# Kernel optimization log

Measured on AMD Instinct MI355X. Metric: run time of the kernel, lower is better.

Reference implementation:

```python
import jax, jax.numpy as jnp
import numpy as np

P = 4          # patch_size
LAM = 0.5      # init_lambda
B, C, H, W = 8, 96, 128, 128

def _dct_mat(N):
    # torch_dct unnormalized DCT-II matrix: D[k,n] = 2*cos(pi*(2n+1)k/(2N))
    n = np.arange(N)
    return 2.0 * np.cos(np.pi * (2.0 * n[None, :] + 1.0) * n[:, None] / (2.0 * N))

_D = jnp.asarray(_dct_mat(P), dtype=jnp.float32)
_Di = jnp.asarray(np.linalg.inv(_dct_mat(P)), dtype=jnp.float32)  # exact inverse -> idct(dct(x)) == x

def _dct2(x):
    # DCT-II over last two dims of [..., P, P]
    return jnp.einsum('ij,...jk,lk->...il', _D, x, _D)

def _idct2(x):
    return jnp.einsum('ij,...jk,lk->...il', _Di, x, _Di)

def _conv3x3(x, w, b):
    y = jax.lax.conv_general_dilated(x, w, (1, 1), 'SAME',
                                     dimension_numbers=('NCHW', 'OIHW', 'NCHW'))
    return y + b[None, :, None, None]

def setup_inputs() -> dict:
    key = jax.random.key(0)
    ks = jax.random.split(key, 5)
    std = 1.0 / np.sqrt(C * 9)
    return {
        'input1': jax.random.normal(ks[0], (B, C, H, W), jnp.float32),
        'input2': jax.random.normal(ks[1], (B, C, H, W), jnp.float32),
        'wq': jax.random.normal(ks[2], (C, C, 3, 3), jnp.float32) * std,
        'bq': jnp.zeros((C,), jnp.float32),
        'wk': jax.random.normal(ks[3], (C, C, 3, 3), jnp.float32) * std,
        'bk': jnp.zeros((C,), jnp.float32),
        'wv': jax.random.normal(ks[4], (C, C, 3, 3), jnp.float32) * std,
        'bv': jnp.zeros((C,), jnp.float32),
        'temperature': jnp.ones((1, 1), jnp.float32),
    }

def reference(input1, input2, wq, bq, wk, bk, wv, bv, temperature):
    b, c, h, w = input1.shape
    F_Q = _conv3x3(input1, wq, bq)
    F_K = _conv3x3(input1, wk, bk)
    F_V = _conv3x3(input2, wv, bv)
    hp, wp = h // P, w // P
    # 'b c (h p1) (w p2) -> b c h w p1 p2'
    to_patch = lambda x: x.reshape(b, c, hp, P, wp, P).transpose(0, 1, 2, 4, 3, 5)
    fft_Q = _dct2(to_patch(F_Q))          # [b,c,hp,wp,P,P]
    fft_K = _dct2(to_patch(F_K))
    F1 = jnp.matmul(fft_Q, fft_K)         # per-patch PxP matmul
    L = hp * wp * P * P                   # == h*w
    F1f = F1.reshape(b, c, L)
    Fq = fft_Q.reshape(b, c, L)
    Fk = fft_K.reshape(b, c, L)
    # channel-channel attention: [b,c,L] @ [b,L,c] -> [b,c,c]
    attn = jnp.einsum('bil,bjl->bij', Fq, Fk) * temperature[0, 0]
    attn = jax.nn.softmax(attn, axis=-1)
    Fcfr = jnp.einsum('bij,bjl->bil', attn, F1f).reshape(b, c, hp, wp, P, P)
    Fcfr_out = _idct2(Fcfr)
    # 'b c h w p1 p2 -> b c (h p1) (w p2)'
    Fcfrout = Fcfr_out.transpose(0, 1, 2, 4, 3, 5).reshape(b, c, h, w)
    out1 = jnp.matmul(Fcfrout, F_V)       # batched HxW matmul (H==W)
    Fdfr = F_V - out1 * LAM
    return jnp.matmul(Fcfrout, F_Q) + Fdfr
```

## Files before the change

### kernel.cpp

```cpp
#include <hip/hip_runtime.h>

typedef unsigned short u16;
typedef unsigned int u32;
typedef __bf16 bf16x8 __attribute__((ext_vector_type(8)));
typedef float f32x4 __attribute__((ext_vector_type(4)));
typedef int i32x4 __attribute__((ext_vector_type(4)));

#define BATCH 8
#define CH 96
#define HWSZ 16384
#define PADP (130*130*96)

#define OFF_FQ     0ULL
#define OFF_FK     50331648ULL
#define OFF_GT     50331648ULL
#define OFF_FVN    75497472ULL
#define OFF_PAD1H  100663296ULL
#define OFF_F1W    100663296ULL
#define OFF_PART   126621696ULL
#define OFF_PAD1L  126621696ULL
#define OFF_PAD2   152580096ULL
#define OFF_FCFR   152580096ULL
#define OFF_FVB    178538496ULL
#define OFF_ATTNB  203704320ULL
#define OFF_WQK    203851776ULL
#define OFF_WV     204515328ULL
#define WS_NEED    204681216ULL

__device__ __forceinline__ u16 f2bf(float f) {
    u32 u = __builtin_bit_cast(u32, f);
    u += 0x7fffu + ((u >> 16) & 1u);
    return (u16)(u >> 16);
}
__device__ __forceinline__ float bf2f(u16 h) {
    u32 u = ((u32)h) << 16;
    return __builtin_bit_cast(float, u);
}
__device__ __forceinline__ f32x4 mfma16(i32x4 a, i32x4 b, f32x4 c) {
    return __builtin_amdgcn_mfma_f32_16x16x32_bf16(
        __builtin_bit_cast(bf16x8, a), __builtin_bit_cast(bf16x8, b), c, 0, 0, 0);
}
__device__ __forceinline__ void gl_lds16(const u16* g, u16* l) {
    __builtin_amdgcn_global_load_lds(
        (const __attribute__((address_space(1))) unsigned int*)g,
        (__attribute__((address_space(3))) unsigned int*)l, 16, 0, 0);
}

__global__ __launch_bounds__(256) void k_diag(float* __restrict__ out, int n, float val) {
    for (int i = blockIdx.x * 256 + threadIdx.x; i < n; i += gridDim.x * 256) out[i] = val;
}

__global__ __launch_bounds__(256) void k_zhalo(u16* __restrict__ p) {
    size_t base = (size_t)blockIdx.x * PADP;
    for (int i = threadIdx.x; i < 130 * 96; i += 256) {
        p[base + i] = 0;
        p[base + (size_t)129 * 130 * 96 + i] = 0;
    }
    for (int i = threadIdx.x; i < 128 * 2 * 96; i += 256) {
        int row = i / 192, k = i - row * 192;
        int x = (k < 96) ? 0 : 129, c = (k < 96) ? k : k - 96;
        p[base + ((size_t)(row + 1) * 130 + x) * 96 + c] = 0;
    }
}

__global__ __launch_bounds__(256) void k_trans_split(const float* __restrict__ src,
        u16* __restrict__ dh, u16* __restrict__ dl) {
    __shared__ float tile[96][129];
    int b = blockIdx.x >> 7, y = blockIdx.x & 127;
    const float* s = src + (size_t)b * CH * HWSZ + (size_t)y * 128;
    for (int idx = threadIdx.x; idx < CH * 128; idx += 256) {
        int c = idx >> 7, x = idx & 127;
        tile[c][x] = s[(size_t)c * HWSZ + x];
    }
    __syncthreads();
    size_t obase = ((size_t)(b * 130 + y + 1) * 130 + 1) * 96;
    for (int idx = threadIdx.x; idx < 128 * CH; idx += 256) {
        int x = idx / CH, c = idx - x * CH;
        float v = tile[c][x];
        u16 h = f2bf(v);
        dh[obase + idx] = h;
        if (dl) dl[obase + idx] = f2bf(v - bf2f(h));
    }
}

__global__ __launch_bounds__(128) void k_weights_all(const float* __restrict__ wq,
        const float* __restrict__ wk, const float* __restrict__ wv,
        u16* __restrict__ dqk, u16* __restrict__ dv) {
    int co = blockIdx.x;
    if (co < 192) {
        const float* w = (co < 96) ? wq : wk;
        int cs = (co < 96) ? co : co - 96;
        for (int idx = threadIdx.x; idx < 864; idx += 128) {
            int tap = idx / 96, ci = idx - tap * 96;
            int cic = ci >> 5, g = (ci >> 3) & 3, c7 = ci & 7;
            float v = w[((size_t)cs * 96 + ci) * 9 + tap];
            u16 h = f2bf(v), lo = f2bf(v - bf2f(h));
            size_t s = (size_t)(cic * 9 + tap);
            dqk[(((s * 2 + 0) * 4 + g) * 192 + co) * 8 + c7] = h;
            dqk[(((s * 2 + 1) * 4 + g) * 192 + co) * 8 + c7] = lo;
        }
    } else {
        int cs = co - 192;
        for (int idx = threadIdx.x; idx < 864; idx += 128) {
            int tap = idx / 96, ci = idx - tap * 96;
            int cic = ci >> 5, g = (ci >> 3) & 3, c7 = ci & 7;
            float v = wv[((size_t)cs * 96 + ci) * 9 + tap];
            size_t s = (size_t)(cic * 9 + tap);
            dv[((s * 4 + g) * 96 + cs) * 8 + c7] = f2bf(v);
        }
    }
}

__global__ __launch_bounds__(512, 4) void k_convqk6h(
        const u16* __restrict__ ph, const u16* __restrict__ pl,
        const u16* __restrict__ wqk,
        const float* __restrict__ bq, const float* __restrict__ bk,
        float* __restrict__ fq, float* __restrict__ fk, int bbase) {
    __shared__ u16 wbuf[2][12288];
    const int tid = threadIdx.x;
    const int wg = ((blockIdx.x & 7) << 6) | (blockIdx.x >> 3);
    const int b = bbase + (wg >> 7), y = wg & 127;
    const int w = tid >> 6, lane = tid & 63, l15 = lane & 15, g = lane >> 4;
    const int wx = w & 3, wc = w >> 2;
    f32x4 acc[2][6];
#pragma unroll
    for (int mf = 0; mf < 2; mf++)
#pragma unroll
        for (int f = 0; f < 6; f++) acc[mf][f] = (f32x4){0.f, 0.f, 0.f, 0.f};
    {
#pragma unroll
        for (int j = 0; j < 3; j++)
            gl_lds16(wqk + (size_t)(tid + j * 512) * 8, &wbuf[0][(size_t)(tid + j * 512) * 8]);
    }
    i32x4 ah0, ah1, al0, al1;
    {
        size_t ab = ((size_t)(b * 130 + y) * 130 + (wx * 32 + l15)) * 96 + g * 8;
        ah0 = *(const i32x4*)(ph + ab);
        ah1 = *(const i32x4*)(ph + ab + 16 * 96);
        al0 = *(const i32x4*)(pl + ab);
        al1 = *(const i32x4*)(pl + ab + 16 * 96);
    }
    __syncthreads();
    for (int s = 0; s < 27; s++) {
        const int cur = s & 1;
        i32x4 nh0, nh1, nl0, nl1;
        if (s + 1 < 27) {
            const u16* src = wqk + (size_t)(s + 1) * 12288;
#pragma unroll
            for (int j = 0; j < 3; j++)
                gl_lds16(src + (size_t)(tid + j * 512) * 8, &wbuf[cur ^ 1][(size_t)(tid + j * 512) * 8]);
            const int s1 = s + 1;
            const int cic1 = s1 / 9, tap1 = s1 - cic1 * 9;
            const int dy1 = tap1 / 3 - 1, dx1 = tap1 - (tap1 / 3) * 3 - 1;
            size_t ab = ((size_t)(b * 130 + y + 1 + dy1) * 130 + (wx * 32 + l15 + 1 + dx1)) * 96
                      + cic1 * 32 + g * 8;
            nh0 = *(const i32x4*)(ph + ab);
            nh1 = *(const i32x4*)(ph + ab + 16 * 96);
            nl0 = *(const i32x4*)(pl + ab);
            nl1 = *(const i32x4*)(pl + ab + 16 * 96);
        }
#pragma unroll
        for (int f = 0; f < 6; f++) {
            const int cob = wc * 96 + f * 16 + l15;
            i32x4 bh = *(const i32x4*)(&wbuf[cur][((0 + g) * 192 + cob) * 8]);
            i32x4 bl = *(const i32x4*)(&wbuf[cur][((4 + g) * 192 + cob) * 8]);
            acc[0][f] = mfma16(ah0, bh, acc[0][f]);
            acc[0][f] = mfma16(ah0, bl, acc[0][f]);
            acc[0][f] = mfma16(al0, bh, acc[0][f]);
            acc[1][f] = mfma16(ah1, bh, acc[1][f]);
            acc[1][f] = mfma16(ah1, bl, acc[1][f]);
            acc[1][f] = mfma16(al1, bh, acc[1][f]);
        }
        __syncthreads();
        if (s + 1 < 27) { ah0 = nh0; ah1 = nh1; al0 = nl0; al1 = nl1; }
    }
    const float* bias = wc ? bk : bq;
    float* op = wc ? fk : fq;
#pragma unroll
    for (int f = 0; f < 6; f++) {
        const int co = f * 16 + l15;
        const float bb = bias[co];
#pragma unroll
        for (int mf = 0; mf < 2; mf++) {
            const int xp = wx * 32 + mf * 16 + g * 4;
#pragma unroll
            for (int r = 0; r < 4; r++)
                op[((size_t)((b * 128 + y) * 128 + xp + r)) * 96 + co] = acc[mf][f][r] + bb;
        }
    }
}

__global__ __launch_bounds__(512, 4) void k_convqk7h(
        const u16* __restrict__ ph, const u16* __restrict__ pl,
        const u16* __restrict__ wqk,
        const float* __restrict__ bq, const float* __restrict__ bk,
        float* __restrict__ fq, float* __restrict__ fk, int bbase) {
    __shared__ u16 wbuf[2][12288];
    const int tid = threadIdx.x;
    const int wg = ((blockIdx.x & 7) << 6) | (blockIdx.x >> 3);
    const int b = bbase + (wg >> 7), y = wg & 127;
    const int w = tid >> 6, lane = tid & 63, l15 = lane & 15, g = lane >> 4;
    const int qk = w >> 2, coh = (w >> 1) & 1, xh = w & 1;
    const int cob = qk * 96 + coh * 48;
    f32x4 acc[4][3];
#pragma unroll
    for (int mf = 0; mf < 4; mf++)
#pragma unroll
        for (int f = 0; f < 3; f++) acc[mf][f] = (f32x4){0.f, 0.f, 0.f, 0.f};
    {
#pragma unroll
        for (int j = 0; j < 3; j++)
            gl_lds16(wqk + (size_t)(tid + j * 512) * 8, &wbuf[0][(size_t)(tid + j * 512) * 8]);
    }
    i32x4 ah[4], al[4];
    {
        size_t ab = ((size_t)(b * 130 + y) * 130 + (xh * 64 + l15)) * 96 + g * 8;
#pragma unroll
        for (int mf = 0; mf < 4; mf++) {
            ah[mf] = *(const i32x4*)(ph + ab + (size_t)mf * 16 * 96);
            al[mf] = *(const i32x4*)(pl + ab + (size_t)mf * 16 * 96);
        }
    }
    __syncthreads();
    for (int s = 0; s < 27; s++) {
        const int cur = s & 1;
        i32x4 nah[4], nal[4];
        if (s + 1 < 27) {
            const u16* src = wqk + (size_t)(s + 1) * 12288;
#pragma unroll
            for (int j = 0; j < 3; j++)
                gl_lds16(src + (size_t)(tid + j * 512) * 8, &wbuf[cur ^ 1][(size_t)(tid + j * 512) * 8]);
            const int s1 = s + 1;
            const int cic1 = s1 / 9, tap1 = s1 - cic1 * 9;
            const int dy1 = tap1 / 3 - 1, dx1 = tap1 - (tap1 / 3) * 3 - 1;
            size_t ab1 = ((size_t)(b * 130 + y + 1 + dy1) * 130 + (xh * 64 + l15 + 1 + dx1)) * 96
                       + cic1 * 32 + g * 8;
#pragma unroll
            for (int mf = 0; mf < 4; mf++) {
                nah[mf] = *(const i32x4*)(ph + ab1 + (size_t)mf * 16 * 96);
                nal[mf] = *(const i32x4*)(pl + ab1 + (size_t)mf * 16 * 96);
            }
        }
#pragma unroll
        for (int f = 0; f < 3; f++) {
            const int cw = cob + f * 16 + l15;
            i32x4 bh = *(const i32x4*)(&wbuf[cur][((0 + g) * 192 + cw) * 8]);
            i32x4 bl = *(const i32x4*)(&wbuf[cur][((4 + g) * 192 + cw) * 8]);
#pragma unroll
            for (int mf = 0; mf < 4; mf++) {
                acc[mf][f] = mfma16(ah[mf], bh, acc[mf][f]);
                acc[mf][f] = mfma16(ah[mf], bl, acc[mf][f]);
                acc[mf][f] = mfma16(al[mf], bh, acc[mf][f]);
            }
        }
        __syncthreads();
        if (s + 1 < 27) {
#pragma unroll
            for (int mf = 0; mf < 4; mf++) { ah[mf] = nah[mf]; al[mf] = nal[mf]; }
        }
    }
    const float* bias = qk ? bk : bq;
    float* op = qk ? fk : fq;
#pragma unroll
    for (int f = 0; f < 3; f++) {
        const int co = coh * 48 + f * 16 + l15;
        const float bb = bias[co];
#pragma unroll
        for (int mf = 0; mf < 4; mf++) {
            const int xp = xh * 64 + mf * 16 + g * 4;
#pragma unroll
            for (int r = 0; r < 4; r++)
                op[((size_t)((b * 128 + y) * 128 + xp + r)) * 96 + co] = acc[mf][f][r] + bb;
        }
    }
}

__global__ __launch_bounds__(512, 4) void k_convv6(
        const u16* __restrict__ p2, const u16* __restrict__ wv,
        const float* __restrict__ bv, u16* __restrict__ fvb) {
    __shared__ u16 vbuf[2][3072];
    const int tid = threadIdx.x;
    const int wg = ((blockIdx.x & 7) << 7) | (blockIdx.x >> 3);
    const int b = wg >> 7, y = wg & 127;
    const int w = tid >> 6, lane = tid & 63, l15 = lane & 15, g = lane >> 4;
    const int wx = w & 3, wc = w >> 2;
    f32x4 acc[2][3];
#pragma unroll
    for (int mf = 0; mf < 2; mf++)
#pragma unroll
        for (int f = 0; f < 3; f++) acc[mf][f] = (f32x4){0.f, 0.f, 0.f, 0.f};
    if (tid < 384)
        gl_lds16(wv + (size_t)tid * 8, &vbuf[0][(size_t)tid * 8]);
    i32x4 ah0, ah1;
    {
        size_t ab = ((size_t)(b * 130 + y) * 130 + (wx * 32 + l15)) * 96 + g * 8;
        ah0 = *(const i32x4*)(p2 + ab);
        ah1 = *(const i32x4*)(p2 + ab + 16 * 96);
    }
    __syncthreads();
    for (int s = 0; s < 27; s++) {
        const int cur = s & 1;
        i32x4 nh0, nh1;
        if (s + 1 < 27) {
            if (tid < 384)
                gl_lds16(wv + (size_t)(s + 1) * 3072 + (size_t)tid * 8, &vbuf[cur ^ 1][(size_t)tid * 8]);
            const int s1 = s + 1;
            const int cic1 = s1 / 9, tap1 = s1 - cic1 * 9;
            const int dy1 = tap1 / 3 - 1, dx1 = tap1 - (tap1 / 3) * 3 - 1;
            size_t ab = ((size_t)(b * 130 + y + 1 + dy1) * 130 + (wx * 32 + l15 + 1 + dx1)) * 96
                      + cic1 * 32 + g * 8;
            nh0 = *(const i32x4*)(p2 + ab);
            nh1 = *(const i32x4*)(p2 + ab + 16 * 96);
        }
#pragma unroll
        for (int f = 0; f < 3; f++) {
            const int cof = wc * 48 + f * 16 + l15;
            i32x4 bfr = *(const i32x4*)(&vbuf[cur][(g * 96 + cof) * 8]);
            acc[0][f] = mfma16(ah0, bfr, acc[0][f]);
            acc[1][f] = mfma16(ah1, bfr, acc[1][f]);
        }
        __syncthreads();
        if (s + 1 < 27) { ah0 = nh0; ah1 = nh1; }
    }
#pragma unroll
    for (int f = 0; f < 3; f++) {
        const int co = wc * 48 + f * 16 + l15;
        const float bb = bv[co];
#pragma unroll
        for (int mf = 0; mf < 2; mf++) {
            const int xp = wx * 32 + mf * 16 + g * 4;
#pragma unroll
            for (int r = 0; r < 4; r++)
                fvb[((size_t)((b * 128 + y) * 128 + xp + r)) * 96 + co] = f2bf(acc[mf][f][r] + bb);
        }
    }
}

__global__ __launch_bounds__(256) void k_pattn2(
        const float* __restrict__ fq, const float* __restrict__ fk,
        u16* __restrict__ f1w, float* __restrict__ part) {
    __shared__ float qs[96 * 65];
    __shared__ float ks[96 * 65];
    int blk = blockIdx.x;
    int b = blk >> 7, ys = (blk >> 2) & 31, xq = blk & 3;
    int y0 = ys * 4, x0 = xq * 32;
    int tx = threadIdx.x & 15, ty = threadIdx.x >> 4;
    double accD[6][6];
#pragma unroll
    for (int a = 0; a < 6; a++)
#pragma unroll
        for (int bb = 0; bb < 6; bb++) accD[a][bb] = 0.0;
#pragma unroll
    for (int cx = 0; cx < 2; cx++) {
        for (int idx = threadIdx.x; idx < 1536; idx += 256) {
            int p = idx / 24, c0 = (idx - p * 24) * 4;
            int ry = p >> 4, rx = p & 15;
            size_t off = ((size_t)((b * 128 + y0 + ry) * 128 + x0 + cx * 16 + rx)) * 96 + c0;
            f32x4 qv = *(const f32x4*)(fq + off);
            f32x4 kv = *(const f32x4*)(fk + off);
#pragma unroll
            for (int u = 0; u < 4; u++) {
                qs[(c0 + u) * 65 + p] = qv[u];
                ks[(c0 + u) * 65 + p] = kv[u];
            }
        }
        __syncthreads();
        for (int item = threadIdx.x; item < 384; item += 256) {
            int j = item / 96, c = item - j * 96;
            float A[4][4], Bm[4][4];
#pragma unroll
            for (int r = 0; r < 4; r++)
#pragma unroll
                for (int m = 0; m < 4; m++) {
                    A[r][m] = qs[c * 65 + r * 16 + j * 4 + m];
                    Bm[r][m] = ks[c * 65 + r * 16 + j * 4 + m];
                }
            float rsB[4], csB[4], rsA[4], tot = 0.f;
#pragma unroll
            for (int r = 0; r < 4; r++) {
                rsB[r] = Bm[r][0] + Bm[r][1] + Bm[r][2] + Bm[r][3];
                rsA[r] = A[r][0] + A[r][1] + A[r][2] + A[r][3];
                tot += rsB[r];
            }
#pragma unroll
            for (int m = 0; m < 4; m++) csB[m] = Bm[0][m] + Bm[1][m] + Bm[2][m] + Bm[3][m];
#pragma unroll
            for (int r = 0; r < 4; r++)
#pragma unroll
                for (int m = 0; m < 4; m++) {
                    float ab = A[r][0] * Bm[0][m] + A[r][1] * Bm[1][m]
                             + A[r][2] * Bm[2][m] + A[r][3] * Bm[3][m];
                    f1w[((size_t)((b * 128 + y0 + r) * 128 + x0 + cx * 16 + j * 4 + m)) * 96 + c]
                        = f2bf(8.f * ab + 2.f * rsA[r] * csB[m]);
                }
#pragma unroll
            for (int r = 0; r < 4; r++)
#pragma unroll
                for (int m = 0; m < 4; m++)
                    ks[c * 65 + r * 16 + j * 4 + m]
                        = 64.f * Bm[r][m] + 16.f * (rsB[r] + csB[m]) + 4.f * tot;
        }
        __syncthreads();
        float acc[6][6];
#pragma unroll
        for (int a = 0; a < 6; a++)
#pragma unroll
            for (int bb = 0; bb < 6; bb++) acc[a][bb] = 0.f;
        for (int l = 0; l < 64; l++) {
            float qv[6], kv[6];
#pragma unroll
            for (int a = 0; a < 6; a++) qv[a] = qs[(ty + 16 * a) * 65 + l];
#pragma unroll
            for (int bb = 0; bb < 6; bb++) kv[bb] = ks[(tx + 16 * bb) * 65 + l];
#pragma unroll
            for (int a = 0; a < 6; a++)
#pragma unroll
                for (int bb = 0; bb < 6; bb++) acc[a][bb] += qv[a] * kv[bb];
        }
#pragma unroll
        for (int a = 0; a < 6; a++)
#pragma unroll
            for (int bb = 0; bb < 6; bb++) accD[a][bb] += (double)acc[a][bb];
        __syncthreads();
    }
    int s128 = ys * 4 + xq;
#pragma unroll
    for (int a = 0; a < 6; a++)
#pragma unroll
        for (int bb = 0; bb < 6; bb++)
            part[((size_t)((b * 128 + s128) * 96 + ty + 16 * a)) * 96 + tx + 16 * bb]
                = (float)accD[a][bb];
}

__global__ __launch_bounds__(128) void k_softmax(
        const float* __restrict__ part, const float* __restrict__ temp,
        u16* __restrict__ attnb) {
    __shared__ float red[128];
    int b = blockIdx.x / 96, i2 = blockIdx.x - b * 96;
    int j2 = threadIdx.x;
    float v = 0.f;
    if (j2 < 96) {
        double vd = 0.0;
        for (int s = 0; s < 128; s++)
            vd += (double)part[((size_t)((b * 128 + s) * 96 + i2)) * 96 + j2];
        v = (float)vd * temp[0];
    }
    red[j2] = (j2 < 96) ? v : -3.4e38f;
    __syncthreads();
    for (int off = 64; off >= 1; off >>= 1) {
        if (j2 < off) red[j2] = fmaxf(red[j2], red[j2 + off]);
        __syncthreads();
    }
    float mx = red[0];
    __syncthreads();
    float e = (j2 < 96) ? expf(v - mx) : 0.f;
    red[j2] = e;
    __syncthreads();
    for (int off = 64; off >= 1; off >>= 1) {
        if (j2 < off) red[j2] += red[j2 + off];
        __syncthreads();
    }
    float sum = red[0];
    if (j2 < 96) attnb[((size_t)(b * 96) + i2) * 96 + j2] = f2bf(e / sum);
}

__global__ __launch_bounds__(256) void k_gprep(
        const float* __restrict__ fqn, const u16* __restrict__ fvb,
        u16* __restrict__ gt, u16* __restrict__ fvn) {
    __shared__ u16 lg[8 * 32 * 33];
    __shared__ u16 lv[8 * 32 * 33];
    int blk = blockIdx.x;
    int b = blk / 192;
    int r = blk - b * 192;
    int yt = r / 48; r -= yt * 48;
    int xt = r / 12; int cc = r - xt * 12;
    int y0 = yt * 32, x0 = xt * 32, c0 = cc * 8;
    for (int idx = threadIdx.x; idx < 8192; idx += 256) {
        int pix = idx >> 3, cl = idx & 7;
        int yy = pix >> 5, xx = pix & 31;
        size_t off = ((size_t)((b * 128 + y0 + yy) * 128 + x0 + xx)) * 96 + c0 + cl;
        float q = fqn[off];
        float v = bf2f(fvb[off]);
        int la = (cl * 32 + yy) * 33 + xx;
        lg[la] = f2bf(q - 0.5f * v);
        lv[la] = f2bf(v);
    }
    __syncthreads();
    for (int idx = threadIdx.x; idx < 8192; idx += 256) {
        int yy = idx & 31, xl = (idx >> 5) & 31, cl = idx >> 10;
        gt[((size_t)((b * 96 + c0 + cl) * 128 + x0 + xl)) * 128 + y0 + yy] = lg[(cl * 32 + yy) * 33 + xl];
    }
    for (int idx = threadIdx.x; idx < 8192; idx += 256) {
        int xx = idx & 31, yl = (idx >> 5) & 31, cl = idx >> 10;
        fvn[((size_t)((b * 96 + c0 + cl) * 128 + y0 + yl)) * 128 + x0 + xx] = lv[(cl * 32 + yl) * 33 + xx];
    }
}

__global__ __launch_bounds__(256) void k_fcfr2(
        const u16* __restrict__ attnb, const u16* __restrict__ f1w,
        u16* __restrict__ fc) {
    int b = blockIdx.x >> 6, pc = blockIdx.x & 63;
    int lane = threadIdx.x & 63, wv_ = threadIdx.x >> 6;
    int l15 = lane & 15, g = lane >> 4;
    int pbase = pc * 256 + wv_ * 64;
    f32x4 acc[6][4];
#pragma unroll
    for (int m = 0; m < 6; m++)
#pragma unroll
        for (int n = 0; n < 4; n++) acc[m][n] = (f32x4){0.f, 0.f, 0.f, 0.f};
#pragma unroll
    for (int ks = 0; ks < 3; ks++) {
        int k0 = ks * 32 + g * 8;
        i32x4 afr[6];
#pragma unroll
        for (int m = 0; m < 6; m++)
            afr[m] = *(const i32x4*)(attnb + ((size_t)(b * 96 + m * 16 + l15)) * 96 + k0);
#pragma unroll
        for (int n = 0; n < 4; n++) {
            i32x4 bfr = *(const i32x4*)(f1w + ((size_t)(b * 16384 + pbase + n * 16 + l15)) * 96 + k0);
#pragma unroll
            for (int m = 0; m < 6; m++)
                acc[m][n] = mfma16(afr[m], bfr, acc[m][n]);
        }
    }
#pragma unroll
    for (int m = 0; m < 6; m++)
#pragma unroll
        for (int n = 0; n < 4; n++)
#pragma unroll
            for (int r = 0; r < 4; r++) {
                int i2 = m * 16 + g * 4 + r;
                int pix = pbase + n * 16 + l15;
                fc[((size_t)(b * 96 + i2)) * HWSZ + pix] = f2bf(acc[m][n][r]);
            }
}

__global__ __launch_bounds__(256) void k_final(
        const u16* __restrict__ fc, const u16* __restrict__ gt,
        const u16* __restrict__ fvn, float* __restrict__ out) {
    int b = blockIdx.x / 96, c = blockIdx.x - b * 96;
    int lane = threadIdx.x & 63, wv_ = threadIdx.x >> 6;
    int l15 = lane & 15, g = lane >> 4;
    const u16* A = fc + ((size_t)(b * 96 + c)) * HWSZ;
    const u16* Bm = gt + ((size_t)(b * 96 + c)) * HWSZ;
    f32x4 acc[2][8];
#pragma unroll
    for (int mf = 0; mf < 2; mf++)
#pragma unroll
        for (int nf = 0; nf < 8; nf++) acc[mf][nf] = (f32x4){0.f, 0.f, 0.f, 0.f};
#pragma unroll
    for (int kc = 0; kc < 4; kc++) {
        int k0 = kc * 32 + g * 8;
        i32x4 af[2];
#pragma unroll
        for (int mf = 0; mf < 2; mf++)
            af[mf] = *(const i32x4*)(A + (size_t)(wv_ * 32 + mf * 16 + l15) * 128 + k0);
#pragma unroll
        for (int nf = 0; nf < 8; nf++) {
            i32x4 bf = *(const i32x4*)(Bm + (size_t)(nf * 16 + l15) * 128 + k0);
#pragma unroll
            for (int mf = 0; mf < 2; mf++)
                acc[mf][nf] = mfma16(af[mf], bf, acc[mf][nf]);
        }
    }
    const u16* V = fvn + ((size_t)(b * 96 + c)) * HWSZ;
    float* O = out + ((size_t)(b * 96 + c)) * HWSZ;
#pragma unroll
    for (int mf = 0; mf < 2; mf++)
#pragma unroll
        for (int nf = 0; nf < 8; nf++)
#pragma unroll
            for (int r = 0; r < 4; r++) {
                int y = wv_ * 32 + mf * 16 + g * 4 + r;
                int x = nf * 16 + l15;
                O[y * 128 + x] = acc[mf][nf][r] + bf2f(V[y * 128 + x]);
            }
}

extern "C" void kernel_launch(void* const* d_in, const int* in_sizes, int n_in,
                              void* d_out, int out_size, void* d_ws, size_t ws_size,
                              hipStream_t stream) {
    (void)in_sizes; (void)n_in;
    if (ws_size < (size_t)WS_NEED) {
        k_diag<<<2048, 256, 0, stream>>>((float*)d_out, out_size, (float)(ws_size >> 10));
        return;
    }
    const float* in1 = (const float*)d_in[0];
    const float* in2 = (const float*)d_in[1];
    const float* wq  = (const float*)d_in[2];
    const float* bq  = (const float*)d_in[3];
    const float* wk  = (const float*)d_in[4];
    const float* bk  = (const float*)d_in[5];
    const float* wv  = (const float*)d_in[6];
    const float* bv  = (const float*)d_in[7];
    const float* temp = (const float*)d_in[8];
    char* ws = (char*)d_ws;
    float* FQ   = (float*)(ws + OFF_FQ);
    float* FK   = (float*)(ws + OFF_FK);
    u16*  GT    = (u16*)(ws + OFF_GT);
    u16*  FVN   = (u16*)(ws + OFF_FVN);
    u16*  PAD1H = (u16*)(ws + OFF_PAD1H);
    u16*  PAD1L = (u16*)(ws + OFF_PAD1L);
    u16*  PAD2  = (u16*)(ws + OFF_PAD2);
    u16*  F1W   = (u16*)(ws + OFF_F1W);
    float* PART = (float*)(ws + OFF_PART);
    u16*  FCFR  = (u16*)(ws + OFF_FCFR);
    u16*  FVB   = (u16*)(ws + OFF_FVB);
    u16*  ATTNB = (u16*)(ws + OFF_ATTNB);
    u16*  WQK   = (u16*)(ws + OFF_WQK);
    u16*  WV    = (u16*)(ws + OFF_WV);

    k_zhalo<<<24, 256, 0, stream>>>(PAD1H);
    k_trans_split<<<1024, 256, 0, stream>>>(in1, PAD1H, PAD1L);
    k_trans_split<<<1024, 256, 0, stream>>>(in2, PAD2, nullptr);
    k_weights_all<<<288, 128, 0, stream>>>(wq, wk, wv, WQK, WV);
    k_convqk6h<<<512, 512, 0, stream>>>(PAD1H, PAD1L, WQK, bq, bk, FQ, FK, 0);
    k_convqk7h<<<512, 512, 0, stream>>>(PAD1H, PAD1L, WQK, bq, bk, FQ, FK, 4);
    k_convv6<<<1024, 512, 0, stream>>>(PAD2, WV, bv, FVB);
    k_pattn2<<<1024, 256, 0, stream>>>(FQ, FK, F1W, PART);
    k_softmax<<<768, 128, 0, stream>>>(PART, temp, ATTNB);
    k_gprep<<<1536, 256, 0, stream>>>(FQ, FVB, GT, FVN);
    k_fcfr2<<<512, 256, 0, stream>>>(ATTNB, F1W, FCFR);
    k_final<<<768, 256, 0, stream>>>(FCFR, GT, FVN, (float*)d_out);
}
```

Measured before the change: 413.6 us.

## Merge input transposes, rotate conv column order, coarsen patch-attention blocks

```diff
diff --git a/kernel.cpp b/kernel.cpp
--- a/kernel.cpp
+++ b/kernel.cpp
@@ -63,10 +63,16 @@
     }
 }
 
-__global__ __launch_bounds__(256) void k_trans_split(const float* __restrict__ src,
-        u16* __restrict__ dh, u16* __restrict__ dl) {
+__global__ __launch_bounds__(256) void k_trans2(const float* __restrict__ in1,
+        const float* __restrict__ in2, u16* __restrict__ p1h, u16* __restrict__ p1l,
+        u16* __restrict__ p2) {
     __shared__ float tile[96][129];
-    int b = blockIdx.x >> 7, y = blockIdx.x & 127;
+    int which = blockIdx.x >> 10;
+    int blk = blockIdx.x & 1023;
+    const float* src = which ? in2 : in1;
+    u16* dh = which ? p2 : p1h;
+    u16* dl = which ? nullptr : p1l;
+    int b = blk >> 7, y = blk & 127;
     const float* s = src + (size_t)b * CH * HWSZ + (size_t)y * 128;
     for (int idx = threadIdx.x; idx < CH * 128; idx += 256) {
         int c = idx >> 7, x = idx & 127;
@@ -190,7 +196,7 @@
     }
 }
 
-__global__ __launch_bounds__(512, 4) void k_convqk7h(
+__global__ __launch_bounds__(512, 4) void k_convqk6r(
         const u16* __restrict__ ph, const u16* __restrict__ pl,
         const u16* __restrict__ wqk,
         const float* __restrict__ bq, const float* __restrict__ bk,
@@ -200,31 +206,30 @@
     const int wg = ((blockIdx.x & 7) << 6) | (blockIdx.x >> 3);
     const int b = bbase + (wg >> 7), y = wg & 127;
     const int w = tid >> 6, lane = tid & 63, l15 = lane & 15, g = lane >> 4;
-    const int qk = w >> 2, coh = (w >> 1) & 1, xh = w & 1;
-    const int cob = qk * 96 + coh * 48;
-    f32x4 acc[4][3];
-#pragma unroll
-    for (int mf = 0; mf < 4; mf++)
-#pragma unroll
-        for (int f = 0; f < 3; f++) acc[mf][f] = (f32x4){0.f, 0.f, 0.f, 0.f};
+    const int wx = w & 3, wc = w >> 2;
+    const int fo = (w % 3) * 2;
+    f32x4 acc[2][6];
+#pragma unroll
+    for (int mf = 0; mf < 2; mf++)
+#pragma unroll
+        for (int f = 0; f < 6; f++) acc[mf][f] = (f32x4){0.f, 0.f, 0.f, 0.f};
     {
 #pragma unroll
         for (int j = 0; j < 3; j++)
             gl_lds16(wqk + (size_t)(tid + j * 512) * 8, &wbuf[0][(size_t)(tid + j * 512) * 8]);
     }
-    i32x4 ah[4], al[4];
+    i32x4 ah0, ah1, al0, al1;
     {
-        size_t ab = ((size_t)(b * 130 + y) * 130 + (xh * 64 + l15)) * 96 + g * 8;
-#pragma unroll
-        for (int mf = 0; mf < 4; mf++) {
-            ah[mf] = *(const i32x4*)(ph + ab + (size_t)mf * 16 * 96);
-            al[mf] = *(const i32x4*)(pl + ab + (size_t)mf * 16 * 96);
-        }
+        size_t ab = ((size_t)(b * 130 + y) * 130 + (wx * 32 + l15)) * 96 + g * 8;
+        ah0 = *(const i32x4*)(ph + ab);
+        ah1 = *(const i32x4*)(ph + ab + 16 * 96);
+        al0 = *(const i32x4*)(pl + ab);
+        al1 = *(const i32x4*)(pl + ab + 16 * 96);
     }
     __syncthreads();
     for (int s = 0; s < 27; s++) {
         const int cur = s & 1;
-        i32x4 nah[4], nal[4];
+        i32x4 nh0, nh1, nl0, nl1;
         if (s + 1 < 27) {
             const u16* src = wqk + (size_t)(s + 1) * 12288;
 #pragma unroll
@@ -233,41 +238,38 @@
             const int s1 = s + 1;
             const int cic1 = s1 / 9, tap1 = s1 - cic1 * 9;
             const int dy1 = tap1 / 3 - 1, dx1 = tap1 - (tap1 / 3) * 3 - 1;
-            size_t ab1 = ((size_t)(b * 130 + y + 1 + dy1) * 130 + (xh * 64 + l15 + 1 + dx1)) * 96
-                       + cic1 * 32 + g * 8;
-#pragma unroll
-            for (int mf = 0; mf < 4; mf++) {
-                nah[mf] = *(const i32x4*)(ph + ab1 + (size_t)mf * 16 * 96);
-                nal[mf] = *(const i32x4*)(pl + ab1 + (size_t)mf * 16 * 96);
-            }
-        }
-#pragma unroll
-        for (int f = 0; f < 3; f++) {
-            const int cw = cob + f * 16 + l15;
-            i32x4 bh = *(const i32x4*)(&wbuf[cur][((0 + g) * 192 + cw) * 8]);
-            i32x4 bl = *(const i32x4*)(&wbuf[cur][((4 + g) * 192 + cw) * 8]);
-#pragma unroll
-            for (int mf = 0; mf < 4; mf++) {
-                acc[mf][f] = mfma16(ah[mf], bh, acc[mf][f]);
-                acc[mf][f] = mfma16(ah[mf], bl, acc[mf][f]);
-                acc[mf][f] = mfma16(al[mf], bh, acc[mf][f]);
-            }
-        }
-        __syncthreads();
-        if (s + 1 < 27) {
-#pragma unroll
-            for (int mf = 0; mf < 4; mf++) { ah[mf] = nah[mf]; al[mf] = nal[mf]; }
-        }
-    }
-    const float* bias = qk ? bk : bq;
-    float* op = qk ? fk : fq;
-#pragma unroll
-    for (int f = 0; f < 3; f++) {
-        const int co = coh * 48 + f * 16 + l15;
+            size_t ab = ((size_t)(b * 130 + y + 1 + dy1) * 130 + (wx * 32 + l15 + 1 + dx1)) * 96
+                      + cic1 * 32 + g * 8;
+            nh0 = *(const i32x4*)(ph + ab);
+            nh1 = *(const i32x4*)(ph + ab + 16 * 96);
+            nl0 = *(const i32x4*)(pl + ab);
+            nl1 = *(const i32x4*)(pl + ab + 16 * 96);
+        }
+#pragma unroll
+        for (int f0 = 0; f0 < 6; f0++) {
+            int f = f0 + fo; if (f >= 6) f -= 6;
+            const int cob = wc * 96 + f * 16 + l15;
+            i32x4 bh = *(const i32x4*)(&wbuf[cur][((0 + g) * 192 + cob) * 8]);
+            i32x4 bl = *(const i32x4*)(&wbuf[cur][((4 + g) * 192 + cob) * 8]);
+            acc[0][f] = mfma16(ah0, bh, acc[0][f]);
+            acc[0][f] = mfma16(ah0, bl, acc[0][f]);
+            acc[0][f] = mfma16(al0, bh, acc[0][f]);
+            acc[1][f] = mfma16(ah1, bh, acc[1][f]);
+            acc[1][f] = mfma16(ah1, bl, acc[1][f]);
+            acc[1][f] = mfma16(al1, bh, acc[1][f]);
+        }
+        __syncthreads();
+        if (s + 1 < 27) { ah0 = nh0; ah1 = nh1; al0 = nl0; al1 = nl1; }
+    }
+    const float* bias = wc ? bk : bq;
+    float* op = wc ? fk : fq;
+#pragma unroll
+    for (int f = 0; f < 6; f++) {
+        const int co = f * 16 + l15;
         const float bb = bias[co];
 #pragma unroll
-        for (int mf = 0; mf < 4; mf++) {
-            const int xp = xh * 64 + mf * 16 + g * 4;
+        for (int mf = 0; mf < 2; mf++) {
+            const int xp = wx * 32 + mf * 16 + g * 4;
 #pragma unroll
             for (int r = 0; r < 4; r++)
                 op[((size_t)((b * 128 + y) * 128 + xp + r)) * 96 + co] = acc[mf][f][r] + bb;
@@ -336,26 +338,26 @@
     }
 }
 
-__global__ __launch_bounds__(256) void k_pattn2(
+__global__ __launch_bounds__(256) void k_pattn3(
         const float* __restrict__ fq, const float* __restrict__ fk,
         u16* __restrict__ f1w, float* __restrict__ part) {
     __shared__ float qs[96 * 65];
     __shared__ float ks[96 * 65];
     int blk = blockIdx.x;
-    int b = blk >> 7, ys = (blk >> 2) & 31, xq = blk & 3;
-    int y0 = ys * 4, x0 = xq * 32;
+    int b = blk >> 5, ys = (blk >> 2) & 7, xq = blk & 3;
+    int y0 = ys * 16, x0 = xq * 32;
     int tx = threadIdx.x & 15, ty = threadIdx.x >> 4;
     double accD[6][6];
 #pragma unroll
     for (int a = 0; a < 6; a++)
 #pragma unroll
         for (int bb = 0; bb < 6; bb++) accD[a][bb] = 0.0;
-#pragma unroll
-    for (int cx = 0; cx < 2; cx++) {
+    for (int sub = 0; sub < 8; sub++) {
+        int yy0 = y0 + (sub >> 1) * 4, xx0 = x0 + (sub & 1) * 16;
         for (int idx = threadIdx.x; idx < 1536; idx += 256) {
             int p = idx / 24, c0 = (idx - p * 24) * 4;
             int ry = p >> 4, rx = p & 15;
-            size_t off = ((size_t)((b * 128 + y0 + ry) * 128 + x0 + cx * 16 + rx)) * 96 + c0;
+            size_t off = ((size_t)((b * 128 + yy0 + ry) * 128 + xx0 + rx)) * 96 + c0;
             f32x4 qv = *(const f32x4*)(fq + off);
             f32x4 kv = *(const f32x4*)(fk + off);
 #pragma unroll
@@ -390,7 +392,7 @@
                 for (int m = 0; m < 4; m++) {
                     float ab = A[r][0] * Bm[0][m] + A[r][1] * Bm[1][m]
                              + A[r][2] * Bm[2][m] + A[r][3] * Bm[3][m];
-                    f1w[((size_t)((b * 128 + y0 + r) * 128 + x0 + cx * 16 + j * 4 + m)) * 96 + c]
+                    f1w[((size_t)((b * 128 + yy0 + r) * 128 + xx0 + j * 4 + m)) * 96 + c]
                         = f2bf(8.f * ab + 2.f * rsA[r] * csB[m]);
                 }
 #pragma unroll
@@ -423,12 +425,12 @@
             for (int bb = 0; bb < 6; bb++) accD[a][bb] += (double)acc[a][bb];
         __syncthreads();
     }
-    int s128 = ys * 4 + xq;
+    int s32 = ys * 4 + xq;
 #pragma unroll
     for (int a = 0; a < 6; a++)
 #pragma unroll
         for (int bb = 0; bb < 6; bb++)
-            part[((size_t)((b * 128 + s128) * 96 + ty + 16 * a)) * 96 + tx + 16 * bb]
+            part[((size_t)((b * 32 + s32) * 96 + ty + 16 * a)) * 96 + tx + 16 * bb]
                 = (float)accD[a][bb];
 }
 
@@ -441,8 +443,8 @@
     float v = 0.f;
     if (j2 < 96) {
         double vd = 0.0;
-        for (int s = 0; s < 128; s++)
-            vd += (double)part[((size_t)((b * 128 + s) * 96 + i2)) * 96 + j2];
+        for (int s = 0; s < 32; s++)
+            vd += (double)part[((size_t)((b * 32 + s) * 96 + i2)) * 96 + j2];
         v = (float)vd * temp[0];
     }
     red[j2] = (j2 < 96) ? v : -3.4e38f;
@@ -611,13 +613,12 @@
     u16*  WV    = (u16*)(ws + OFF_WV);
 
     k_zhalo<<<24, 256, 0, stream>>>(PAD1H);
-    k_trans_split<<<1024, 256, 0, stream>>>(in1, PAD1H, PAD1L);
-    k_trans_split<<<1024, 256, 0, stream>>>(in2, PAD2, nullptr);
+    k_trans2<<<2048, 256, 0, stream>>>(in1, in2, PAD1H, PAD1L, PAD2);
     k_weights_all<<<288, 128, 0, stream>>>(wq, wk, wv, WQK, WV);
     k_convqk6h<<<512, 512, 0, stream>>>(PAD1H, PAD1L, WQK, bq, bk, FQ, FK, 0);
-    k_convqk7h<<<512, 512, 0, stream>>>(PAD1H, PAD1L, WQK, bq, bk, FQ, FK, 4);
+    k_convqk6r<<<512, 512, 0, stream>>>(PAD1H, PAD1L, WQK, bq, bk, FQ, FK, 4);
     k_convv6<<<1024, 512, 0, stream>>>(PAD2, WV, bv, FVB);
-    k_pattn2<<<1024, 256, 0, stream>>>(FQ, FK, F1W, PART);
+    k_pattn3<<<256, 256, 0, stream>>>(FQ, FK, F1W, PART);
     k_softmax<<<768, 128, 0, stream>>>(PART, temp, ATTNB);
     k_gprep<<<1536, 256, 0, stream>>>(FQ, FVB, GT, FVN);
     k_fcfr2<<<512, 256, 0, stream>>>(ATTNB, F1W, FCFR);
```

After: 790.9 us. +91.2%, slower.
